# Optimization experiments

Hardware: AMD Instinct MI355X
Metric: run time of the kernel (lower is better)

Reference implementation:

```python
import jax, jax.numpy as jnp
import numpy as np
import math

B, S, D, H, M = 2, 2048, 1024, 16, 64
HD = D // H  # head_dim = 64


def setup_inputs() -> dict:
    key = jax.random.key(0)
    ks = jax.random.split(key, 16)
    inp = {
        "query": jax.random.normal(ks[0], (B, S, D), jnp.float32),
        "key": jax.random.normal(ks[1], (B, S, D), jnp.float32),
        "value": jax.random.normal(ks[2], (B, S, D), jnp.float32),
        "mask": jax.random.randint(ks[3], (B, 1, 1, S), 0, 2, jnp.int32),
        "Wq": jax.random.normal(ks[4], (D, D), jnp.float32) * 0.02,
        "bq": jnp.zeros((D,), jnp.float32),
        "Wk": jax.random.normal(ks[5], (D, D), jnp.float32) * 0.02,
        "bk": jnp.zeros((D,), jnp.float32),
        "Wv": jax.random.normal(ks[6], (D, D), jnp.float32) * 0.02,
        "bv": jnp.zeros((D,), jnp.float32),
        "Wo": jax.random.normal(ks[7], (D, D), jnp.float32) * 0.02,
        "bo": jnp.zeros((D,), jnp.float32),
        "m_k": jax.random.normal(ks[8], (1, M, D), jnp.float32) * (1.0 / HD),
        "m_v": jax.random.normal(ks[9], (1, M, D), jnp.float32) * (1.0 / M),
    }
    return inp


def reference(query, key, value, mask, Wq, bq, Wk, bk, Wv, bv, Wo, bo, m_k, m_v):
    b, nq, d = query.shape
    nk = key.shape[1]
    h, hd, m = H, HD, M
    scale = math.sqrt(hd)

    Q = query @ Wq.T + bq                      # [b, nq, d]
    K = key @ Wk.T + bk                        # [b, nk, d]
    V = value @ Wv.T + bv                      # [b, nk, d]

    mk = scale * jnp.broadcast_to(m_k, (b, m, d))           # sqrt(head_dim)*m_k
    mv = math.sqrt(m) * jnp.broadcast_to(m_v, (b, m, d))    # sqrt(m)*m_v

    K = jnp.concatenate([K, mk], axis=1)       # [b, nk+m, d]
    V = jnp.concatenate([V, mv], axis=1)

    Qh = Q.reshape(b, nq, h, hd).transpose(0, 2, 1, 3)           # [b,h,nq,hd]
    Kh = K.reshape(b, nk + m, h, hd).transpose(0, 2, 1, 3)       # [b,h,nk+m,hd]
    Vh = V.reshape(b, nk + m, h, hd).transpose(0, 2, 1, 3)

    energy = jnp.einsum('bhqd,bhkd->bhqk', Qh, Kh) / scale       # [b,h,nq,nk+m]
    # mask only the first nk key columns; memory slots are never masked
    masked = jnp.where(mask == 0, jnp.float32(-1e20), energy[..., :nk])
    energy = jnp.concatenate([masked, energy[..., nk:]], axis=-1)

    attention = jax.nn.softmax(energy, axis=-1)
    x = jnp.einsum('bhqk,bhkd->bhqd', attention, Vh)             # [b,h,nq,hd]
    x = x.transpose(0, 2, 1, 3).reshape(b, nq, d)
    return x @ Wo.T + bo
```

## Files before the change

kernel.cpp:

```cpp
#include <hip/hip_runtime.h>
#include <hip/hip_bf16.h>
#include <stdint.h>

#define B_  2
#define S_  2048
#define D_  1024
#define H_  16
#define HD_ 64
#define M_  64
#define SKM (S_ + M_)
#define LOG2E 1.44269504088896340736f

typedef __attribute__((ext_vector_type(8))) short s16x8;
typedef __attribute__((ext_vector_type(4))) float f32x4;
typedef __attribute__((ext_vector_type(16))) float f32x16;

#define GLOAD16(gp, lp) __builtin_amdgcn_global_load_lds( \
    (const __attribute__((address_space(1))) void*)(gp),  \
    (__attribute__((address_space(3))) void*)(lp), 16, 0, 0)

#define WAITVM(N) do { asm volatile("s_waitcnt vmcnt(" #N ")" ::: "memory"); \
                       __builtin_amdgcn_sched_barrier(0); } while (0)
#define BARRIER() do { asm volatile("" ::: "memory"); \
                       __builtin_amdgcn_s_barrier(); \
                       asm volatile("" ::: "memory"); } while (0)

__device__ __forceinline__ unsigned short f2bf(float f) {
  union { float f; unsigned int u; } v; v.f = f;
  unsigned int r = v.u + 0x7fffu + ((v.u >> 16) & 1u);
  return (unsigned short)(r >> 16);
}

__device__ __forceinline__ unsigned pkbf(float lo, float hi) {
  union { __hip_bfloat162 b; unsigned u; } t;
  t.b = __float22bfloat162_rn(make_float2(lo, hi));
  return t.u;
}

__global__ void compact_mask(const int* __restrict__ mask,
                             int* __restrict__ idx, int* __restrict__ cnt) {
  const int b = blockIdx.x;
  __shared__ int base, wsum[4];
  if (threadIdx.x == 0) base = 0;
  const int lane = threadIdx.x & 63, w = threadIdx.x >> 6;
  __syncthreads();
  for (int c = 0; c < S_; c += 256) {
    int key = c + threadIdx.x;
    int mv = mask[b * S_ + key];
    unsigned long long bal = __ballot(mv != 0);
    int pre = __popcll(bal & ((1ull << lane) - 1ull));
    if (lane == 0) wsum[w] = __popcll(bal);
    __syncthreads();
    int woff = 0;
    for (int i = 0; i < w; i++) woff += wsum[i];
    int tot = wsum[0] + wsum[1] + wsum[2] + wsum[3];
    if (mv) idx[b * S_ + base + woff + pre] = key;
    __syncthreads();
    if (threadIdx.x == 0) base += tot;
    __syncthreads();
  }
  if (threadIdx.x == 0) cnt[b] = base;
}

__global__ void cvt_fused(const float* __restrict__ q,
                          const float* __restrict__ w0, const float* __restrict__ w1,
                          const float* __restrict__ w2, const float* __restrict__ w3,
                          const float* __restrict__ key, const float* __restrict__ value,
                          unsigned short* __restrict__ qf,
                          unsigned short* __restrict__ o0, unsigned short* __restrict__ o1,
                          unsigned short* __restrict__ o2, unsigned short* __restrict__ o3,
                          unsigned short* __restrict__ kf, unsigned short* __restrict__ vf,
                          const int* __restrict__ idx, const int* __restrict__ cnt) {
  const size_t NQs = (size_t)B_ * S_ * D_;
  if (blockIdx.x < 8192) {
    size_t i = ((size_t)blockIdx.x * 256 + threadIdx.x) * 4;
    const float* in; unsigned short* out; size_t off;
    if (i < NQs) { in = q; out = qf; off = i; }
    else {
      size_t j = i - NQs;
      int wsel = (int)(j >> 20);
      off = j & ((1u << 20) - 1);
      in  = (wsel == 0) ? w0 : (wsel == 1) ? w1 : (wsel == 2) ? w2 : w3;
      out = (wsel == 0) ? o0 : (wsel == 1) ? o1 : (wsel == 2) ? o2 : o3;
    }
    float4 v = *(const float4*)&in[off];
    ushort4 o;
    o.x = f2bf(v.x); o.y = f2bf(v.y); o.z = f2bf(v.z); o.w = f2bf(v.w);
    *(ushort4*)&out[off] = o;
  } else {
    int gid = blockIdx.x - 8192;
    int kv = gid >> 12, rem = gid & 4095;
    int b = rem >> 11, j = rem & 2047;
    if (j >= cnt[b]) return;
    const float* in = kv ? value : key;
    unsigned short* out = kv ? vf : kf;
    int src = idx[b * S_ + j];
    const float* ip = in + ((size_t)(b * S_) + src) * D_;
    unsigned short* op = out + ((size_t)(b * S_) + j) * D_;
    int t = threadIdx.x * 4;
    float4 v = *(const float4*)&ip[t];
    ushort4 o;
    o.x = f2bf(v.x); o.y = f2bf(v.y); o.z = f2bf(v.z); o.w = f2bf(v.w);
    *(ushort4*)&op[t] = o;
  }
}

__global__ void fill_mem(const float* __restrict__ mk, const float* __restrict__ mv,
                         unsigned short* __restrict__ Kb, unsigned short* __restrict__ VtG,
                         const int* __restrict__ cnt) {
  int i = blockIdx.x * 256 + threadIdx.x;
  int row = i >> 10, col = i & 1023;
  int hI = col >> 6, dd = col & 63;
  unsigned short kv = f2bf(8.0f * mk[i]);
  unsigned short vv = f2bf(8.0f * mv[i]);
#pragma unroll
  for (int b = 0; b < B_; b++) {
    int c = cnt[b];
    Kb[((size_t)(b * SKM) + c + row) * D_ + col] = kv;
    VtG[((size_t)(b * H_ + hI) * HD_ + dd) * SKM + c + row] = vv;
  }
}

__device__ __forceinline__ void gemm_core3(
    const unsigned short* __restrict__ A,
    const unsigned short* __restrict__ Bw,
    unsigned short* As, unsigned short* Bs,
    int mBase, int nBase, int K,
    int tid, f32x4 acc[4][2]) {
  const int lane = tid & 63, w = tid >> 6;
  const int wr = w >> 2, wc = w & 3;
  const int lr = lane & 15, lk = lane >> 4;
  const int srow = tid >> 2;
  const int cd = tid & 3;
  const int ca = cd ^ ((srow >> 1) & 3);
  const int NT = K / 32;

#define STAGE_(buf, k0)                                                          \
  {                                                                              \
    GLOAD16(&A[(size_t)(mBase + srow) * K + (k0) + ca * 8],                      \
            &As[(buf) * (128 * 32) + (w * 16) * 32]);                            \
    GLOAD16(&Bw[(size_t)(nBase + srow) * K + (k0) + ca * 8],                     \
            &Bs[(buf) * (128 * 32) + (w * 16) * 32]);                            \
  }

  STAGE_(0, 0);
  STAGE_(1, 32);
  int cur = 0;
  for (int t = 0; t < NT; ++t) {
    if (t + 2 < NT) {
      int stg = cur ? cur - 1 : 2;
      STAGE_(stg, (t + 2) * 32);
      WAITVM(4);
    } else if (t + 2 == NT) {
      WAITVM(2);
    } else {
      WAITVM(0);
    }
    BARRIER();
    s16x8 af[4], bf[2];
#pragma unroll
    for (int mi = 0; mi < 4; mi++) {
      int row = wr * 64 + mi * 16 + lr;
      af[mi] = *(const s16x8*)&As[cur * (128 * 32) + row * 32 + ((lk ^ ((row >> 1) & 3)) << 3)];
    }
#pragma unroll
    for (int ni = 0; ni < 2; ni++) {
      int row = wc * 32 + ni * 16 + lr;
      bf[ni] = *(const s16x8*)&Bs[cur * (128 * 32) + row * 32 + ((lk ^ ((row >> 1) & 3)) << 3)];
    }
#pragma unroll
    for (int mi = 0; mi < 4; mi++)
#pragma unroll
      for (int ni = 0; ni < 2; ni++)
        acc[mi][ni] = __builtin_amdgcn_mfma_f32_16x16x32_bf16(af[mi], bf[ni], acc[mi][ni], 0, 0, 0);
    BARRIER();
    cur = (cur == 2) ? 0 : cur + 1;
  }
#undef STAGE_
}

__global__ __launch_bounds__(512)
void gemm_qkv(const unsigned short* __restrict__ qf, const unsigned short* __restrict__ kf,
              const unsigned short* __restrict__ vf,
              const unsigned short* __restrict__ wq, const unsigned short* __restrict__ wk,
              const unsigned short* __restrict__ wv,
              const float* __restrict__ bq, const float* __restrict__ bk,
              const float* __restrict__ bv,
              unsigned short* __restrict__ Qb, unsigned short* __restrict__ Kb,
              unsigned short* __restrict__ Vt,
              const int* __restrict__ cnt) {
  __shared__ __align__(16) unsigned short As[3 * 128 * 32];
  __shared__ __align__(16) unsigned short Bs[3 * 128 * 32];
  const int z = blockIdx.x >> 8;
  const int local = blockIdx.x & 255;
  const int wsz = (local & 7) * 32 + (local >> 3);
  const int nBase = (wsz & 7) * 128, mBase = (wsz >> 3) * 128;
  const int bb = (mBase >= S_);
  if (z) {
    if (mBase - bb * S_ >= cnt[bb]) return;
  }
  const unsigned short* A  = (z == 0) ? qf : (z == 1) ? kf : vf;
  const unsigned short* Bw = (z == 0) ? wq : (z == 1) ? wk : wv;
  const float* bias        = (z == 0) ? bq : (z == 1) ? bk : bv;

  const int tid = threadIdx.x, lane = tid & 63;
  const int w = tid >> 6, wr = w >> 2, wc = w & 3;
  const int lr = lane & 15, lk = lane >> 4;

  const f32x4 fz = {0.f, 0.f, 0.f, 0.f};
  f32x4 acc[4][2];
#pragma unroll
  for (int i = 0; i < 4; i++)
#pragma unroll
    for (int j = 0; j < 2; j++) acc[i][j] = fz;

  gemm_core3(A, Bw, As, Bs, mBase, nBase, D_, tid, acc);

  const float alpha = (z == 0) ? 0.125f * LOG2E : 1.0f;
#pragma unroll
  for (int mi = 0; mi < 4; mi++)
#pragma unroll
    for (int ni = 0; ni < 2; ni++)
#pragma unroll
      for (int r = 0; r < 4; r++) {
        int gr = mBase + wr * 64 + mi * 16 + lk * 4 + r;
        int gc = nBase + wc * 32 + ni * 16 + lr;
        float v = (acc[mi][ni][r] + bias[gc]) * alpha;
        if (z == 2) {
          int s = gr - bb * S_;
          int hI = gc >> 6, dd = gc & 63;
          Vt[((size_t)(bb * H_ + hI) * HD_ + dd) * SKM + s] = f2bf(v);
        } else if (z == 1) {
          int orow = gr + bb * M_;
          Kb[(size_t)orow * D_ + gc] = f2bf(v);
        } else {
          Qb[(size_t)gr * D_ + gc] = f2bf(v);
        }
      }
}

__global__ __launch_bounds__(512)
void gemm_o(const unsigned short* __restrict__ A, const unsigned short* __restrict__ Bw,
            const float* __restrict__ bias, float* __restrict__ Cout) {
  __shared__ __align__(16) unsigned short As[3 * 128 * 32];
  __shared__ __align__(16) unsigned short Bs[3 * 128 * 32];
  const int local = blockIdx.x & 255;
  const int wsz = (local & 7) * 32 + (local >> 3);
  const int nBase = (wsz & 7) * 128, mBase = (wsz >> 3) * 128;
  const int tid = threadIdx.x, lane = tid & 63;
  const int w = tid >> 6, wr = w >> 2, wc = w & 3;
  const int lr = lane & 15, lk = lane >> 4;

  const f32x4 fz = {0.f, 0.f, 0.f, 0.f};
  f32x4 acc[4][2];
#pragma unroll
  for (int i = 0; i < 4; i++)
#pragma unroll
    for (int j = 0; j < 2; j++) acc[i][j] = fz;

  gemm_core3(A, Bw, As, Bs, mBase, nBase, D_, tid, acc);

#pragma unroll
  for (int mi = 0; mi < 4; mi++)
#pragma unroll
    for (int ni = 0; ni < 2; ni++)
#pragma unroll
      for (int r = 0; r < 4; r++) {
        int gr = mBase + wr * 64 + mi * 16 + lk * 4 + r;
        int gc = nBase + wc * 32 + ni * 16 + lr;
        Cout[(size_t)gr * D_ + gc] = acc[mi][ni][r] + bias[gc];
      }
}

__global__ __launch_bounds__(512)
void attn_kernel(const unsigned short* __restrict__ Qb,
                 const unsigned short* __restrict__ Kb,
                 const unsigned short* __restrict__ VtG,
                 const int* __restrict__ cnt,
                 unsigned short* __restrict__ Xb) {
  __shared__ __align__(16) unsigned short Ks[64 * 64];
  __shared__ __align__(16) unsigned short Vs[64 * 64];

  const int tid = threadIdx.x, lane = tid & 63, w = tid >> 6;
  const int l31 = lane & 31, hh = lane >> 5;
  const int qt = blockIdx.x, h = blockIdx.y, b = blockIdx.z;

  const int total = cnt[b] + M_;
  const int nt = (total + 63) >> 6;

  const int r0 = tid >> 3, c0 = tid & 7;
  const int ck = c0 ^ (r0 & 7);
  const unsigned short* Kg = Kb + (size_t)b * SKM * D_ + (size_t)h * HD_;
  const unsigned short* Vg = VtG + (size_t)(b * H_ + h) * HD_ * SKM;

  const unsigned short* qp = Qb + ((size_t)(b * S_) + qt * 256 + w * 32 + l31) * D_ + h * HD_;
  s16x8 qf[4];
#pragma unroll
  for (int ds = 0; ds < 4; ds++) qf[ds] = *(const s16x8*)&qp[ds * 16 + hh * 8];

  f32x16 accO[2];
#pragma unroll
  for (int dt = 0; dt < 2; dt++)
#pragma unroll
    for (int j = 0; j < 16; j++) accO[dt][j] = 0.f;
  float m_r = -1e20f, l_r = 0.f;

  uint4 kr0, vr0;
  auto LOAD = [&](int kt) {
    kr0 = *(const uint4*)&Kg[(size_t)(kt * 64 + r0) * D_ + c0 * 8];
    vr0 = *(const uint4*)&Vg[(size_t)r0 * SKM + kt * 64 + c0 * 8];
  };
  LOAD(0);

  for (int kt = 0; kt < nt; ++kt) {
    __syncthreads();
    *(uint4*)&Ks[r0 * 64 + ck * 8] = kr0;
    *(uint4*)&Vs[r0 * 64 + ck * 8] = vr0;
    __syncthreads();
    if (kt + 1 < nt) LOAD(kt + 1);

    f32x16 p0, p1;
#pragma unroll
    for (int j = 0; j < 16; j++) { p0[j] = 0.f; p1[j] = 0.f; }
    __builtin_amdgcn_s_setprio(1);
#pragma unroll
    for (int ds = 0; ds < 4; ds++) {
      s16x8 ka0 = *(const s16x8*)&Ks[l31 * 64 + (((ds * 2 + hh) ^ (l31 & 7)) << 3)];
      s16x8 ka1 = *(const s16x8*)&Ks[(32 + l31) * 64 + (((ds * 2 + hh) ^ (l31 & 7)) << 3)];
      p0 = __builtin_amdgcn_mfma_f32_32x32x16_bf16(ka0, qf[ds], p0, 0, 0, 0);
      p1 = __builtin_amdgcn_mfma_f32_32x32x16_bf16(ka1, qf[ds], p1, 0, 0, 0);
    }
    __builtin_amdgcn_s_setprio(0);

    if (kt == nt - 1) {
      int valid = total - kt * 64;
#pragma unroll
      for (int j = 0; j < 16; j++) {
        int kl = (j & 3) + 8 * (j >> 2) + 4 * hh;
        if (kl >= valid) p0[j] = -1e30f;
        if (kl + 32 >= valid) p1[j] = -1e30f;
      }
    }

    float vmax = fmaxf(p0[0], p1[0]);
#pragma unroll
    for (int j = 1; j < 16; j++) vmax = fmaxf(vmax, fmaxf(p0[j], p1[j]));
    vmax = fmaxf(vmax, __shfl_xor(vmax, 32));
    if (!__all(vmax - m_r <= 8.0f)) {
      float mnew = fmaxf(m_r, vmax);
      float fac = __builtin_amdgcn_exp2f(m_r - mnew);
      m_r = mnew;
      l_r *= fac;
#pragma unroll
      for (int dt = 0; dt < 2; dt++)
#pragma unroll
        for (int j = 0; j < 16; j++) accO[dt][j] *= fac;
    }
    float sum = 0.f;
#pragma unroll
    for (int j = 0; j < 16; j++) {
      p0[j] = __builtin_amdgcn_exp2f(p0[j] - m_r); sum += p0[j];
      p1[j] = __builtin_amdgcn_exp2f(p1[j] - m_r); sum += p1[j];
    }
    sum += __shfl_xor(sum, 32);
    l_r += sum;

    s16x8 pf_[4];
#pragma unroll
    for (int ks = 0; ks < 4; ks++) {
      const int base = (ks & 1) * 8;
#define ELT(t) ((ks >= 2) ? p1[base + (t)] : p0[base + (t)])
      unsigned w0 = pkbf(ELT(0), ELT(1));
      unsigned w1 = pkbf(ELT(2), ELT(3));
      unsigned w2 = pkbf(ELT(4), ELT(5));
      unsigned w3 = pkbf(ELT(6), ELT(7));
#undef ELT
      unsigned s0 = hh ? w0 : w2;
      unsigned s1 = hh ? w1 : w3;
      unsigned g0 = (unsigned)__shfl_xor((int)s0, 32);
      unsigned g1 = (unsigned)__shfl_xor((int)s1, 32);
      union { s16x8 v; unsigned u[4]; } pf;
      pf.u[0] = hh ? g0 : w0;
      pf.u[1] = hh ? g1 : w1;
      pf.u[2] = hh ? w2 : g0;
      pf.u[3] = hh ? w3 : g1;
      pf_[ks] = pf.v;
    }

    __builtin_amdgcn_s_setprio(1);
#pragma unroll
    for (int dt = 0; dt < 2; dt++)
#pragma unroll
      for (int ks = 0; ks < 4; ks++) {
        s16x8 va = *(const s16x8*)&Vs[(dt * 32 + l31) * 64 + (((ks * 2 + hh) ^ (l31 & 7)) << 3)];
        accO[dt] = __builtin_amdgcn_mfma_f32_32x32x16_bf16(va, pf_[ks], accO[dt], 0, 0, 0);
      }
    __builtin_amdgcn_s_setprio(0);
  }

  float invl = 1.0f / l_r;
  size_t orow = ((size_t)(b * S_) + qt * 256 + w * 32 + l31) * D_ + h * HD_;
#pragma unroll
  for (int dt = 0; dt < 2; dt++)
#pragma unroll
    for (int j = 0; j < 16; j++) {
      int d = dt * 32 + (j & 3) + 8 * (j >> 2) + 4 * hh;
      Xb[orow + d] = f2bf(accO[dt][j] * invl);
    }
}

extern "C" void kernel_launch(void* const* d_in, const int* in_sizes, int n_in,
                              void* d_out, int out_size, void* d_ws, size_t ws_size,
                              hipStream_t stream) {
  const float* query = (const float*)d_in[0];
  const float* key   = (const float*)d_in[1];
  const float* value = (const float*)d_in[2];
  const int*   mask  = (const int*)d_in[3];
  const float* Wq    = (const float*)d_in[4];
  const float* bq    = (const float*)d_in[5];
  const float* Wk    = (const float*)d_in[6];
  const float* bk    = (const float*)d_in[7];
  const float* Wv    = (const float*)d_in[8];
  const float* bv    = (const float*)d_in[9];
  const float* Wo    = (const float*)d_in[10];
  const float* bo    = (const float*)d_in[11];
  const float* m_k   = (const float*)d_in[12];
  const float* m_v   = (const float*)d_in[13];

  const int NQ = B_ * S_ * D_;
  const int NW = D_ * D_;
  const int NK = B_ * SKM * D_;

  unsigned short* ws = (unsigned short*)d_ws;
  unsigned short* qf = ws;
  unsigned short* kf = qf + NQ;
  unsigned short* vf = kf + NQ;
  unsigned short* wq = vf + NQ;
  unsigned short* wk = wq + NW;
  unsigned short* wv = wk + NW;
  unsigned short* wo = wv + NW;
  unsigned short* Qb = wo + NW;
  unsigned short* Kb = Qb + NQ;
  unsigned short* Vt = Kb + NK;
  unsigned short* Xb = Vt + NK;
  int* idx = (int*)(Xb + NQ);
  int* cnt = idx + B_ * S_;

  compact_mask<<<B_, 256, 0, stream>>>(mask, idx, cnt);
  cvt_fused<<<16384, 256, 0, stream>>>(query, Wq, Wk, Wv, Wo, key, value,
                                       qf, wq, wk, wv, wo, kf, vf, idx, cnt);

  gemm_qkv<<<768, 512, 0, stream>>>(qf, kf, vf, wq, wk, wv, bq, bk, bv, Qb, Kb, Vt, cnt);
  fill_mem<<<(M_ * D_) / 256, 256, 0, stream>>>(m_k, m_v, Kb, Vt, cnt);

  attn_kernel<<<dim3(S_ / 256, H_, B_), 512, 0, stream>>>(Qb, Kb, Vt, cnt, Xb);

  gemm_o<<<256, 512, 0, stream>>>(Xb, wo, bo, (float*)d_out);
}
```

Measured before the change: 127.0 us.

## Double-buffer attention K/V tiles, single-barrier GEMM pipeline, fuse memory-slot fill

The attention kernel now double-buffers its K/V tiles in LDS. The next tile is stored into the alternate buffer after compute, so each iteration needs one barrier instead of two. The QKV and output GEMMs drop the trailing barrier and prefetch one stage ahead across a 3-buffer ring. The separate fill_mem launch is folded into gemm_qkv as 16 extra blocks, and K/V epilogue writes are now guarded by the compacted count so they cannot overwrite the memory-slot rows filled concurrently. This trades extra LDS and a shallower GEMM prefetch for fewer syncs and one fewer launch.

```diff
diff --git a/kernel.cpp b/kernel.cpp
--- a/kernel.cpp
+++ b/kernel.cpp
@@ -105,80 +105,6 @@
   }
 }
 
-__global__ void fill_mem(const float* __restrict__ mk, const float* __restrict__ mv,
-                         unsigned short* __restrict__ Kb, unsigned short* __restrict__ VtG,
-                         const int* __restrict__ cnt) {
-  int i = blockIdx.x * 256 + threadIdx.x;
-  int row = i >> 10, col = i & 1023;
-  int hI = col >> 6, dd = col & 63;
-  unsigned short kv = f2bf(8.0f * mk[i]);
-  unsigned short vv = f2bf(8.0f * mv[i]);
-#pragma unroll
-  for (int b = 0; b < B_; b++) {
-    int c = cnt[b];
-    Kb[((size_t)(b * SKM) + c + row) * D_ + col] = kv;
-    VtG[((size_t)(b * H_ + hI) * HD_ + dd) * SKM + c + row] = vv;
-  }
-}
-
-__device__ __forceinline__ void gemm_core3(
-    const unsigned short* __restrict__ A,
-    const unsigned short* __restrict__ Bw,
-    unsigned short* As, unsigned short* Bs,
-    int mBase, int nBase, int K,
-    int tid, f32x4 acc[4][2]) {
-  const int lane = tid & 63, w = tid >> 6;
-  const int wr = w >> 2, wc = w & 3;
-  const int lr = lane & 15, lk = lane >> 4;
-  const int srow = tid >> 2;
-  const int cd = tid & 3;
-  const int ca = cd ^ ((srow >> 1) & 3);
-  const int NT = K / 32;
-
-#define STAGE_(buf, k0)                                                          \
-  {                                                                              \
-    GLOAD16(&A[(size_t)(mBase + srow) * K + (k0) + ca * 8],                      \
-            &As[(buf) * (128 * 32) + (w * 16) * 32]);                            \
-    GLOAD16(&Bw[(size_t)(nBase + srow) * K + (k0) + ca * 8],                     \
-            &Bs[(buf) * (128 * 32) + (w * 16) * 32]);                            \
-  }
-
-  STAGE_(0, 0);
-  STAGE_(1, 32);
-  int cur = 0;
-  for (int t = 0; t < NT; ++t) {
-    if (t + 2 < NT) {
-      int stg = cur ? cur - 1 : 2;
-      STAGE_(stg, (t + 2) * 32);
-      WAITVM(4);
-    } else if (t + 2 == NT) {
-      WAITVM(2);
-    } else {
-      WAITVM(0);
-    }
-    BARRIER();
-    s16x8 af[4], bf[2];
-#pragma unroll
-    for (int mi = 0; mi < 4; mi++) {
-      int row = wr * 64 + mi * 16 + lr;
-      af[mi] = *(const s16x8*)&As[cur * (128 * 32) + row * 32 + ((lk ^ ((row >> 1) & 3)) << 3)];
-    }
-#pragma unroll
-    for (int ni = 0; ni < 2; ni++) {
-      int row = wc * 32 + ni * 16 + lr;
-      bf[ni] = *(const s16x8*)&Bs[cur * (128 * 32) + row * 32 + ((lk ^ ((row >> 1) & 3)) << 3)];
-    }
-#pragma unroll
-    for (int mi = 0; mi < 4; mi++)
-#pragma unroll
-      for (int ni = 0; ni < 2; ni++)
-        acc[mi][ni] = __builtin_amdgcn_mfma_f32_16x16x32_bf16(af[mi], bf[ni], acc[mi][ni], 0, 0, 0);
-    BARRIER();
-    cur = (cur == 2) ? 0 : cur + 1;
-  }
-#undef STAGE_
-}
-
 __global__ __launch_bounds__(512)
 void gemm_qkv(const unsigned short* __restrict__ qf, const unsigned short* __restrict__ kf,
               const unsigned short* __restrict__ vf,
@@ -186,26 +112,53 @@
               const unsigned short* __restrict__ wv,
               const float* __restrict__ bq, const float* __restrict__ bk,
               const float* __restrict__ bv,
+              const float* __restrict__ mk, const float* __restrict__ mv,
               unsigned short* __restrict__ Qb, unsigned short* __restrict__ Kb,
               unsigned short* __restrict__ Vt,
-              const int* __restrict__ cnt) {
+              const int* __restrict__ idx, const int* __restrict__ cnt) {
   __shared__ __align__(16) unsigned short As[3 * 128 * 32];
   __shared__ __align__(16) unsigned short Bs[3 * 128 * 32];
+
+  if (blockIdx.x >= 768) {
+    int fb = blockIdx.x - 768;
+#pragma unroll
+    for (int k = 0; k < 8; k++) {
+      int i = fb * 4096 + k * 512 + threadIdx.x;
+      int row = i >> 10, col = i & 1023;
+      int hI = col >> 6, dd = col & 63;
+      unsigned short kvv = f2bf(8.0f * mk[i]);
+      unsigned short vvv = f2bf(8.0f * mv[i]);
+#pragma unroll
+      for (int b = 0; b < B_; b++) {
+        int c = cnt[b];
+        Kb[((size_t)(b * SKM) + c + row) * D_ + col] = kvv;
+        Vt[((size_t)(b * H_ + hI) * HD_ + dd) * SKM + c + row] = vvv;
+      }
+    }
+    return;
+  }
+
   const int z = blockIdx.x >> 8;
   const int local = blockIdx.x & 255;
   const int wsz = (local & 7) * 32 + (local >> 3);
   const int nBase = (wsz & 7) * 128, mBase = (wsz >> 3) * 128;
   const int bb = (mBase >= S_);
+  const int climit = z ? cnt[bb] : S_;
   if (z) {
-    if (mBase - bb * S_ >= cnt[bb]) return;
+    if (mBase - bb * S_ >= climit) return;
   }
   const unsigned short* A  = (z == 0) ? qf : (z == 1) ? kf : vf;
   const unsigned short* Bw = (z == 0) ? wq : (z == 1) ? wk : wv;
   const float* bias        = (z == 0) ? bq : (z == 1) ? bk : bv;
 
   const int tid = threadIdx.x, lane = tid & 63;
-  const int w = tid >> 6, wr = w >> 2, wc = w & 3;
+  const int w = tid >> 6;
+  const int wr = w >> 2, wc = w & 3;
   const int lr = lane & 15, lk = lane >> 4;
+  const int srow = tid >> 2;
+  const int cd = tid & 3;
+  const int ca = cd ^ ((srow >> 1) & 3);
+  const int NT = D_ / 32;
 
   const f32x4 fz = {0.f, 0.f, 0.f, 0.f};
   f32x4 acc[4][2];
@@ -214,7 +167,44 @@
 #pragma unroll
     for (int j = 0; j < 2; j++) acc[i][j] = fz;
 
-  gemm_core3(A, Bw, As, Bs, mBase, nBase, D_, tid, acc);
+#define STAGE_(buf, k0)                                                          \
+  {                                                                              \
+    GLOAD16(&A[(size_t)(mBase + srow) * D_ + (k0) + ca * 8],                     \
+            &As[(buf) * (128 * 32) + (w * 16) * 32]);                            \
+    GLOAD16(&Bw[(size_t)(nBase + srow) * D_ + (k0) + ca * 8],                    \
+            &Bs[(buf) * (128 * 32) + (w * 16) * 32]);                            \
+  }
+
+  STAGE_(0, 0);
+  int cur = 0;
+  for (int t = 0; t < NT; ++t) {
+    if (t + 1 < NT) {
+      int nb = (cur == 2) ? 0 : cur + 1;
+      STAGE_(nb, (t + 1) * 32);
+      WAITVM(2);
+    } else {
+      WAITVM(0);
+    }
+    BARRIER();
+    s16x8 af[4], bf[2];
+#pragma unroll
+    for (int mi = 0; mi < 4; mi++) {
+      int row = wr * 64 + mi * 16 + lr;
+      af[mi] = *(const s16x8*)&As[cur * (128 * 32) + row * 32 + ((lk ^ ((row >> 1) & 3)) << 3)];
+    }
+#pragma unroll
+    for (int ni = 0; ni < 2; ni++) {
+      int row = wc * 32 + ni * 16 + lr;
+      bf[ni] = *(const s16x8*)&Bs[cur * (128 * 32) + row * 32 + ((lk ^ ((row >> 1) & 3)) << 3)];
+    }
+#pragma unroll
+    for (int mi = 0; mi < 4; mi++)
+#pragma unroll
+      for (int ni = 0; ni < 2; ni++)
+        acc[mi][ni] = __builtin_amdgcn_mfma_f32_16x16x32_bf16(af[mi], bf[ni], acc[mi][ni], 0, 0, 0);
+    cur = (cur == 2) ? 0 : cur + 1;
+  }
+#undef STAGE_
 
   const float alpha = (z == 0) ? 0.125f * LOG2E : 1.0f;
 #pragma unroll
@@ -228,11 +218,16 @@
         float v = (acc[mi][ni][r] + bias[gc]) * alpha;
         if (z == 2) {
           int s = gr - bb * S_;
-          int hI = gc >> 6, dd = gc & 63;
-          Vt[((size_t)(bb * H_ + hI) * HD_ + dd) * SKM + s] = f2bf(v);
+          if (s < climit) {
+            int hI = gc >> 6, dd = gc & 63;
+            Vt[((size_t)(bb * H_ + hI) * HD_ + dd) * SKM + s] = f2bf(v);
+          }
         } else if (z == 1) {
-          int orow = gr + bb * M_;
-          Kb[(size_t)orow * D_ + gc] = f2bf(v);
+          int rr = gr - bb * S_;
+          if (rr < climit) {
+            int orow = gr + bb * M_;
+            Kb[(size_t)orow * D_ + gc] = f2bf(v);
+          }
         } else {
           Qb[(size_t)gr * D_ + gc] = f2bf(v);
         }
@@ -248,8 +243,13 @@
   const int wsz = (local & 7) * 32 + (local >> 3);
   const int nBase = (wsz & 7) * 128, mBase = (wsz >> 3) * 128;
   const int tid = threadIdx.x, lane = tid & 63;
-  const int w = tid >> 6, wr = w >> 2, wc = w & 3;
+  const int w = tid >> 6;
+  const int wr = w >> 2, wc = w & 3;
   const int lr = lane & 15, lk = lane >> 4;
+  const int srow = tid >> 2;
+  const int cd = tid & 3;
+  const int ca = cd ^ ((srow >> 1) & 3);
+  const int NT = D_ / 32;
 
   const f32x4 fz = {0.f, 0.f, 0.f, 0.f};
   f32x4 acc[4][2];
@@ -258,7 +258,44 @@
 #pragma unroll
     for (int j = 0; j < 2; j++) acc[i][j] = fz;
 
-  gemm_core3(A, Bw, As, Bs, mBase, nBase, D_, tid, acc);
+#define STAGE_(buf, k0)                                                          \
+  {                                                                              \
+    GLOAD16(&A[(size_t)(mBase + srow) * D_ + (k0) + ca * 8],                     \
+            &As[(buf) * (128 * 32) + (w * 16) * 32]);                            \
+    GLOAD16(&Bw[(size_t)(nBase + srow) * D_ + (k0) + ca * 8],                    \
+            &Bs[(buf) * (128 * 32) + (w * 16) * 32]);                            \
+  }
+
+  STAGE_(0, 0);
+  int cur = 0;
+  for (int t = 0; t < NT; ++t) {
+    if (t + 1 < NT) {
+      int nb = (cur == 2) ? 0 : cur + 1;
+      STAGE_(nb, (t + 1) * 32);
+      WAITVM(2);
+    } else {
+      WAITVM(0);
+    }
+    BARRIER();
+    s16x8 af[4], bf[2];
+#pragma unroll
+    for (int mi = 0; mi < 4; mi++) {
+      int row = wr * 64 + mi * 16 + lr;
+      af[mi] = *(const s16x8*)&As[cur * (128 * 32) + row * 32 + ((lk ^ ((row >> 1) & 3)) << 3)];
+    }
+#pragma unroll
+    for (int ni = 0; ni < 2; ni++) {
+      int row = wc * 32 + ni * 16 + lr;
+      bf[ni] = *(const s16x8*)&Bs[cur * (128 * 32) + row * 32 + ((lk ^ ((row >> 1) & 3)) << 3)];
+    }
+#pragma unroll
+    for (int mi = 0; mi < 4; mi++)
+#pragma unroll
+      for (int ni = 0; ni < 2; ni++)
+        acc[mi][ni] = __builtin_amdgcn_mfma_f32_16x16x32_bf16(af[mi], bf[ni], acc[mi][ni], 0, 0, 0);
+    cur = (cur == 2) ? 0 : cur + 1;
+  }
+#undef STAGE_
 
 #pragma unroll
   for (int mi = 0; mi < 4; mi++)
@@ -278,8 +315,8 @@
                  const unsigned short* __restrict__ VtG,
                  const int* __restrict__ cnt,
                  unsigned short* __restrict__ Xb) {
-  __shared__ __align__(16) unsigned short Ks[64 * 64];
-  __shared__ __align__(16) unsigned short Vs[64 * 64];
+  __shared__ __align__(16) unsigned short Ks[2 * 64 * 64];
+  __shared__ __align__(16) unsigned short Vs[2 * 64 * 64];
 
   const int tid = threadIdx.x, lane = tid & 63, w = tid >> 6;
   const int l31 = lane & 31, hh = lane >> 5;
@@ -310,23 +347,27 @@
     kr0 = *(const uint4*)&Kg[(size_t)(kt * 64 + r0) * D_ + c0 * 8];
     vr0 = *(const uint4*)&Vg[(size_t)r0 * SKM + kt * 64 + c0 * 8];
   };
+
   LOAD(0);
+  *(uint4*)&Ks[r0 * 64 + ck * 8] = kr0;
+  *(uint4*)&Vs[r0 * 64 + ck * 8] = vr0;
+  __syncthreads();
+  int cur = 0;
 
   for (int kt = 0; kt < nt; ++kt) {
-    __syncthreads();
-    *(uint4*)&Ks[r0 * 64 + ck * 8] = kr0;
-    *(uint4*)&Vs[r0 * 64 + ck * 8] = vr0;
-    __syncthreads();
-    if (kt + 1 < nt) LOAD(kt + 1);
-
+    const bool pre = (kt + 1 < nt);
+    if (pre) LOAD(kt + 1);
+
+    const unsigned short* Kc = &Ks[cur * 4096];
+    const unsigned short* Vc = &Vs[cur * 4096];
     f32x16 p0, p1;
 #pragma unroll
     for (int j = 0; j < 16; j++) { p0[j] = 0.f; p1[j] = 0.f; }
     __builtin_amdgcn_s_setprio(1);
 #pragma unroll
     for (int ds = 0; ds < 4; ds++) {
-      s16x8 ka0 = *(const s16x8*)&Ks[l31 * 64 + (((ds * 2 + hh) ^ (l31 & 7)) << 3)];
-      s16x8 ka1 = *(const s16x8*)&Ks[(32 + l31) * 64 + (((ds * 2 + hh) ^ (l31 & 7)) << 3)];
+      s16x8 ka0 = *(const s16x8*)&Kc[l31 * 64 + (((ds * 2 + hh) ^ (l31 & 7)) << 3)];
+      s16x8 ka1 = *(const s16x8*)&Kc[(32 + l31) * 64 + (((ds * 2 + hh) ^ (l31 & 7)) << 3)];
       p0 = __builtin_amdgcn_mfma_f32_32x32x16_bf16(ka0, qf[ds], p0, 0, 0, 0);
       p1 = __builtin_amdgcn_mfma_f32_32x32x16_bf16(ka1, qf[ds], p1, 0, 0, 0);
     }
@@ -392,10 +433,17 @@
     for (int dt = 0; dt < 2; dt++)
 #pragma unroll
       for (int ks = 0; ks < 4; ks++) {
-        s16x8 va = *(const s16x8*)&Vs[(dt * 32 + l31) * 64 + (((ks * 2 + hh) ^ (l31 & 7)) << 3)];
+        s16x8 va = *(const s16x8*)&Vc[(dt * 32 + l31) * 64 + (((ks * 2 + hh) ^ (l31 & 7)) << 3)];
         accO[dt] = __builtin_amdgcn_mfma_f32_32x32x16_bf16(va, pf_[ks], accO[dt], 0, 0, 0);
       }
     __builtin_amdgcn_s_setprio(0);
+
+    if (pre) {
+      *(uint4*)&Ks[(cur ^ 1) * 4096 + r0 * 64 + ck * 8] = kr0;
+      *(uint4*)&Vs[(cur ^ 1) * 4096 + r0 * 64 + ck * 8] = vr0;
+      __syncthreads();
+      cur ^= 1;
+    }
   }
 
   float invl = 1.0f / l_r;
@@ -450,8 +498,8 @@
   cvt_fused<<<16384, 256, 0, stream>>>(query, Wq, Wk, Wv, Wo, key, value,
                                        qf, wq, wk, wv, wo, kf, vf, idx, cnt);
 
-  gemm_qkv<<<768, 512, 0, stream>>>(qf, kf, vf, wq, wk, wv, bq, bk, bv, Qb, Kb, Vt, cnt);
-  fill_mem<<<(M_ * D_) / 256, 256, 0, stream>>>(m_k, m_v, Kb, Vt, cnt);
+  gemm_qkv<<<784, 512, 0, stream>>>(qf, kf, vf, wq, wk, wv, bq, bk, bv,
+                                    m_k, m_v, Qb, Kb, Vt, idx, cnt);
 
   attn_kernel<<<dim3(S_ / 256, H_, B_), 512, 0, stream>>>(Qb, Kb, Vt, cnt, Xb);
 
```

After: 127.3 us. No clear change (+0.2%).
